# Kernel tuning notes

Measured on AMD Instinct MI355X. Metric: run time of the kernel, lower is better.

The kernel has to match this reference:

```python
import jax, jax.numpy as jnp
import numpy as np

N = 50000      # nodes (single node type 'tx')
E = 400000     # edges per edge type ('fwd' and 'rev')
F_IN = 128     # input feature dim
F = 128        # cfg.gnn.dim_inner
H = 8          # attention heads
D = F // H     # per-head dim
L = 2          # cfg.gnn.layers_mp
C = 2          # dim_out (fraud logits)


def setup_inputs() -> dict:
    key = jax.random.key(0)
    k = jax.random.split(key, 12)
    f32 = jnp.float32
    g = lambda kk, sh, fan: jax.random.normal(kk, sh, f32) / np.float32(np.sqrt(fan))
    return dict(
        x=jax.random.normal(k[0], (N, F_IN), f32),
        edge_index_fwd=jax.random.randint(k[1], (2, E), 0, N),
        edge_index_rev=jax.random.randint(k[2], (2, E), 0, N),
        in_w=g(k[3], (F_IN, F), F_IN),
        in_b=jnp.zeros((F,), f32),
        kqv_w=g(k[4], (L, F, 3 * F), F),
        kqv_b=jnp.zeros((L, 3 * F), f32),
        krel_w=g(k[5], (L, 2, H, D, D), D),
        vrel_w=g(k[6], (L, 2, H, D, D), D),
        p_rel=jnp.ones((L, 2, H), f32),
        out_w=g(k[7], (L, F, F), F),
        out_b=jnp.zeros((L, F), f32),
        skip=jnp.ones((L,), f32),
        head_w=g(k[8], (F, C), F),
        head_b=jnp.zeros((C,), f32),
    )


def reference(x, edge_index_fwd, edge_index_rev, in_w, in_b, kqv_w, kqv_b,
              krel_w, vrel_w, p_rel, out_w, out_b, skip, head_w, head_b):
    n = x.shape[0]
    ef, er = edge_index_fwd, edge_index_rev
    Ef, Er = ef.shape[1], er.shape[1]
    dst = jnp.concatenate([ef[1], er[1]])                 # [E_tot]
    scale = 1.0 / jnp.sqrt(jnp.asarray(D, x.dtype))

    h = x @ in_w + in_b                                   # in_proj['tx'], [N,F]
    for l in range(L):
        kqv = h @ kqv_w[l] + kqv_b[l]                     # [N,3F]
        k, q, v = jnp.split(kqv, 3, axis=1)
        k = k.reshape(n, H, D)
        q = q.reshape(n, H, D)
        v = v.reshape(n, H, D)
        # per-edge-type relation transforms (head-wise DxD, no bias)
        k_rel = jnp.einsum('nhd,ehdf->enhf', k, krel_w[l])  # [2,N,H,D]
        v_rel = jnp.einsum('nhd,ehdf->enhf', v, vrel_w[l])
        # gather src features per edge type, concatenate edge types
        k_j = jnp.concatenate([k_rel[0][ef[0]], k_rel[1][er[0]]], axis=0)  # [E_tot,H,D]
        v_j = jnp.concatenate([v_rel[0][ef[0]], v_rel[1][er[0]]], axis=0)
        p_e = jnp.concatenate([jnp.broadcast_to(p_rel[l, 0], (Ef, H)),
                               jnp.broadcast_to(p_rel[l, 1], (Er, H))], axis=0)
        q_i = q[dst]                                       # [E_tot,H,D]
        alpha = jnp.einsum('ehd,ehd->eh', q_i, k_j) * p_e * scale
        # segment softmax over all incoming edges of each dst node
        m = jax.ops.segment_max(alpha, dst, num_segments=n)
        ex = jnp.exp(alpha - m[dst])
        denom = jax.ops.segment_sum(ex, dst, num_segments=n)
        w = ex / (denom[dst] + 1e-16)                      # [E_tot,H]
        agg = jax.ops.segment_sum(w[:, :, None] * v_j, dst,
                                  num_segments=n).reshape(n, F)
        a = jax.nn.gelu(agg, approximate=False) @ out_w[l] + out_b[l]
        g = jax.nn.sigmoid(skip[l])
        h = jax.nn.relu(g * a + (1.0 - g) * h)             # skip + act(dropout=0)
    return h @ head_w + head_b                             # logits [N,C]
```

## Files before the change

kernel.cpp:

```cpp
#include <hip/hip_runtime.h>
#include <math.h>

typedef short short8 __attribute__((ext_vector_type(8)));
typedef float f32x4 __attribute__((ext_vector_type(4)));

__device__ __forceinline__ unsigned short f2bf(float f){
    unsigned u = __float_as_uint(f);
    unsigned r = u + 0x7fffu + ((u >> 16) & 1u);
    return (unsigned short)(r >> 16);
}
__device__ __forceinline__ float bf2f(unsigned short s){
    return __uint_as_float((unsigned)s << 16);
}

__global__ void k_count(const int* __restrict__ ef, const int* __restrict__ er,
                        int* __restrict__ deg, int Ef, int Er)
{
    int Etot = Ef + Er;
    for (int e = blockIdx.x*blockDim.x + threadIdx.x; e < Etot; e += gridDim.x*blockDim.x) {
        int dst = (e < Ef) ? ef[Ef + e] : er[Er + (e - Ef)];
        atomicAdd(&deg[dst], 1);
    }
}

__global__ void k_chunk_sums(const int* __restrict__ deg, int* __restrict__ csum, int n)
{
    __shared__ int s[256];
    int t = threadIdx.x, i = blockIdx.x*256 + t;
    s[t] = (i < n) ? deg[i] : 0;
    __syncthreads();
    for (int off = 128; off > 0; off >>= 1) {
        if (t < off) s[t] += s[t + off];
        __syncthreads();
    }
    if (t == 0) csum[blockIdx.x] = s[0];
}

__global__ void k_scan_chunks(int* __restrict__ csum, int nch)
{
    __shared__ int s[1024];
    int t = threadIdx.x;
    int v = (t < nch) ? csum[t] : 0;
    s[t] = v; __syncthreads();
    for (int off = 1; off < 1024; off <<= 1) {
        int u = (t >= off) ? s[t - off] : 0;
        __syncthreads();
        s[t] += u;
        __syncthreads();
    }
    if (t < nch) csum[t] = s[t] - v;
}

__global__ void k_rowstart(const int* __restrict__ deg, const int* __restrict__ csum,
                           int* __restrict__ row_start, int* __restrict__ cursor, int n)
{
    __shared__ int s[256];
    int t = threadIdx.x, i = blockIdx.x*256 + t;
    int d = (i < n) ? deg[i] : 0;
    s[t] = d; __syncthreads();
    for (int off = 1; off < 256; off <<= 1) {
        int u = (t >= off) ? s[t - off] : 0;
        __syncthreads();
        s[t] += u;
        __syncthreads();
    }
    if (i <= n) {
        int rs = csum[blockIdx.x] + s[t] - d;
        row_start[i] = rs;
        cursor[i] = rs;
    }
}

__global__ void k_fill(const int* __restrict__ ef, const int* __restrict__ er,
                       int* __restrict__ cursor, unsigned* __restrict__ srcs,
                       int Ef, int Er, int n_nodes)
{
    int Etot = Ef + Er;
    if (blockIdx.x == 0 && threadIdx.x < 8) srcs[Etot + threadIdx.x] = 0;
    for (int e = blockIdx.x*blockDim.x + threadIdx.x; e < Etot; e += gridDim.x*blockDim.x) {
        int src, dst, tt;
        if (e < Ef) { src = ef[e]; dst = ef[Ef + e]; tt = 0; }
        else { int e2 = e - Ef; src = er[e2]; dst = er[Er + e2]; tt = 1; }
        int pos = atomicAdd(&cursor[dst], 1);
        srcs[pos] = (unsigned)(tt*n_nodes + src)*32u;
    }
}

__global__ void k_setup(const float* __restrict__ kqv_w, const float* __restrict__ kqv_b,
                        const float* __restrict__ krel_w, const float* __restrict__ vrel_w,
                        const float* __restrict__ p_rel, const float* __restrict__ out_w,
                        const float* __restrict__ out_b, const float* __restrict__ in_w,
                        const float* __restrict__ x, const float* __restrict__ head_b,
                        unsigned short* __restrict__ WcT, float* __restrict__ biasc,
                        unsigned short* __restrict__ WoT, float* __restrict__ biaso,
                        unsigned short* __restrict__ WiT, unsigned short* __restrict__ x16,
                        int* __restrict__ deg, float* __restrict__ logits, int n_nodes)
{
    const int N0 = 2*129*640;
    const int N1 = N0 + 2*129*128;
    const int N2 = N1 + 128*128;
    const long long N3 = (long long)N2 + (long long)n_nodes*32;
    const long long N4 = N3 + n_nodes;
    const long long N5 = N4 + 2*n_nodes;

    for (long long idx = (long long)blockIdx.x*blockDim.x + threadIdx.x; idx < N5;
         idx += (long long)gridDim.x*blockDim.x) {
        if (idx < N0) {
            int i = (int)idx;
            int l = i / (129*640);
            int rem = i % (129*640);
            int r = rem / 640, c = rem % 640;
            float val;
            if (c < 128) {
                val = (r < 128) ? kqv_w[((size_t)l*128 + r)*384 + 128 + c]
                                : kqv_b[l*384 + 128 + c];
            } else {
                int c2 = c - 128;
                int tt = c2 >> 8;
                int cc = c2 & 255;
                int f = cc >> 1;
                int part = cc & 1;
                int hh = f >> 4, fd = f & 15;
                const float* rw = (part == 0 ? krel_w : vrel_w)
                                  + (((size_t)(l*2 + tt)*8 + hh)*16)*16 + fd;
                int base_col = (part == 0 ? 0 : 256) + hh*16;
                float s = 0.f;
                #pragma unroll
                for (int d = 0; d < 16; ++d) {
                    float a = (r < 128) ? kqv_w[((size_t)l*128 + r)*384 + base_col + d]
                                        : kqv_b[l*384 + base_col + d];
                    s += a * rw[d*16];
                }
                if (part == 0) s *= p_rel[(l*2 + tt)*8 + hh] * 0.25f * 1.4426950408889634f;
                val = s;
            }
            if (r < 128) WcT[((size_t)l*640 + c)*128 + r] = f2bf(val);
            else         biasc[l*640 + c] = val;
        } else if (idx < N1) {
            int i = (int)(idx - N0);
            int l = i / (129*128);
            int rem = i % (129*128);
            int r = rem / 128, c = rem % 128;
            if (r < 128) WoT[((size_t)l*128 + c)*128 + r] = f2bf(out_w[((size_t)l*128 + r)*128 + c]);
            else         biaso[l*128 + c] = out_b[l*128 + c];
        } else if (idx < N2) {
            int i = (int)(idx - N1);
            int r = i >> 7, c = i & 127;
            WiT[(size_t)c*128 + r] = f2bf(in_w[(size_t)r*128 + c]);
        } else if (idx < N3) {
            long long i = idx - N2;
            float4 v = *(const float4*)&x[i*4];
            uint2 w;
            w.x = (unsigned)f2bf(v.x) | ((unsigned)f2bf(v.y) << 16);
            w.y = (unsigned)f2bf(v.z) | ((unsigned)f2bf(v.w) << 16);
            *(uint2*)&x16[i*4] = w;
        } else if (idx < N4) {
            deg[idx - N3] = 0;
        } else {
            long long i = idx - N4;
            logits[i] = head_b[i & 1];
        }
    }
}

__global__ __launch_bounds__(256) void k_mfma(
    const unsigned short* __restrict__ A16, const unsigned short* __restrict__ WT,
    const float* __restrict__ biasc, unsigned short* __restrict__ q16,
    unsigned short* __restrict__ h16, unsigned* __restrict__ kv,
    const float* __restrict__ skip, const float* __restrict__ hw,
    float* __restrict__ logits, int l,
    int n_nodes, int R, int C, int mode)
{
    __shared__ uint4 As[64*16];
    __shared__ uint4 Ws[64*16];
    int b = blockIdx.x;
    int xcd = b & 7, jj = b >> 3;
    int r_t = (jj / C)*8 + xcd;
    int c_t = jj % C;
    if (r_t >= R) return;
    int n0 = r_t*64, c0 = c_t*64;
    int t = threadIdx.x;

    #pragma unroll
    for (int it = 0; it < 4; ++it) {
        int gi = t + it*256;
        int m = gi >> 4, g = gi & 15;
        uint4 a = *(const uint4*)&A16[((size_t)(n0 + m)*16 + g)*8];
        As[m*16 + (g ^ (m & 15))] = a;
    }
    #pragma unroll
    for (int it = 0; it < 4; ++it) {
        int gi = t + it*256;
        int cw = gi >> 4, g = gi & 15;
        uint4 wv = *(const uint4*)&WT[((size_t)(c0 + cw)*16 + g)*8];
        Ws[cw*16 + (g ^ (cw & 15))] = wv;
    }
    __syncthreads();

    int lane = t & 63, w = t >> 6;
    int lm = lane & 15, quad = lane >> 4;
    f32x4 acc[4];
    #pragma unroll
    for (int i = 0; i < 4; ++i) { acc[i][0]=0.f; acc[i][1]=0.f; acc[i][2]=0.f; acc[i][3]=0.f; }

    #pragma unroll
    for (int chunk = 0; chunk < 4; ++chunk) {
        int gq = chunk*4 + quad;
        short8 bfrag = *(const short8*)&Ws[(w*16 + lm)*16 + (gq ^ lm)];
        #pragma unroll
        for (int i = 0; i < 4; ++i) {
            short8 afrag = *(const short8*)&As[(i*16 + lm)*16 + (gq ^ lm)];
            acc[i] = __builtin_amdgcn_mfma_f32_16x16x32_bf16(afrag, bfrag, acc[i], 0, 0, 0);
        }
    }

    int c = c0 + w*16 + lm;
    float bc = biasc[c];
    bool even = (lane & 1) == 0;
    if (mode == 3) {
        float g = 1.f/(1.f + expf(-skip[l]));
        float hw0 = hw[c*2], hw1 = hw[c*2 + 1];
        #pragma unroll
        for (int i = 0; i < 4; ++i) {
            #pragma unroll
            for (int rr = 0; rr < 4; ++rr) {
                int m = n0 + i*16 + quad*4 + rr;
                float nv = 0.f;
                if (m < n_nodes) {
                    float hv = bf2f(h16[(size_t)m*128 + c]);
                    nv = fmaxf(g*(acc[i][rr] + bc) + (1.f - g)*hv, 0.f);
                }
                float p0 = nv*hw0, p1 = nv*hw1;
                p0 += __shfl_xor(p0, 1); p1 += __shfl_xor(p1, 1);
                p0 += __shfl_xor(p0, 2); p1 += __shfl_xor(p1, 2);
                p0 += __shfl_xor(p0, 4); p1 += __shfl_xor(p1, 4);
                p0 += __shfl_xor(p0, 8); p1 += __shfl_xor(p1, 8);
                if (lm == 0 && m < n_nodes) {
                    atomicAdd(&logits[m*2],     p0);
                    atomicAdd(&logits[m*2 + 1], p1);
                }
            }
        }
    } else if (mode == 2) {
        float g = 1.f/(1.f + expf(-skip[l]));
        unsigned* dst = (unsigned*)h16;
        #pragma unroll
        for (int i = 0; i < 4; ++i) {
            #pragma unroll
            for (int rr = 0; rr < 4; ++rr) {
                int m = n0 + i*16 + quad*4 + rr;
                float hv = (m < n_nodes) ? bf2f(h16[(size_t)m*128 + c]) : 0.f;
                float nv = fmaxf(g*(acc[i][rr] + bc) + (1.f - g)*hv, 0.f);
                float other = __shfl_xor(nv, 1);
                if (even && m < n_nodes)
                    dst[(size_t)m*64 + (c >> 1)] =
                        (unsigned)f2bf(nv) | ((unsigned)f2bf(other) << 16);
            }
        }
    } else if (mode == 0) {
        unsigned* dst = (unsigned*)h16;
        #pragma unroll
        for (int i = 0; i < 4; ++i) {
            #pragma unroll
            for (int rr = 0; rr < 4; ++rr) {
                int m = n0 + i*16 + quad*4 + rr;
                float nv = acc[i][rr] + bc;
                float other = __shfl_xor(nv, 1);
                if (even && m < n_nodes)
                    dst[(size_t)m*64 + (c >> 1)] =
                        (unsigned)f2bf(nv) | ((unsigned)f2bf(other) << 16);
            }
        }
    } else if (c0 < 128) {
        unsigned* dst = (unsigned*)q16;
        #pragma unroll
        for (int i = 0; i < 4; ++i) {
            #pragma unroll
            for (int rr = 0; rr < 4; ++rr) {
                float val = acc[i][rr] + bc;
                float other = __shfl_xor(val, 1);
                int m = n0 + i*16 + quad*4 + rr;
                if (even && m < n_nodes)
                    dst[(size_t)m*64 + (c >> 1)] =
                        (unsigned)f2bf(val) | ((unsigned)f2bf(other) << 16);
            }
        }
    } else {
        int c2 = c - 128;
        int tt = c2 >> 8;
        int f = (c2 & 255) >> 1;
        unsigned* dst = kv + (size_t)tt*n_nodes*128;
        #pragma unroll
        for (int i = 0; i < 4; ++i) {
            #pragma unroll
            for (int rr = 0; rr < 4; ++rr) {
                float val = acc[i][rr] + bc;
                float other = __shfl_xor(val, 1);
                int m = n0 + i*16 + quad*4 + rr;
                if (even && m < n_nodes) {
                    unsigned wd = ((unsigned)f2bf(val) << 16) | (unsigned)f2bf(other);
                    dst[(size_t)m*128 + f] = wd;
                }
            }
        }
    }
}

__global__ __launch_bounds__(256) void k_attn(
    const unsigned* __restrict__ srcs, const int* __restrict__ row_start,
    const uint4* __restrict__ kv, const unsigned short* __restrict__ q16,
    unsigned short* __restrict__ qa16, int n_nodes)
{
    int lane = threadIdx.x & 31;
    int n = blockIdx.x*8 + (threadIdx.x >> 5);
    if (n >= n_nodes) return;
    uint2 qp = *(const uint2*)&q16[(size_t)n*128 + lane*4];
    float4 q4;
    q4.x = __uint_as_float(qp.x << 16);
    q4.y = __uint_as_float(qp.x & 0xffff0000u);
    q4.z = __uint_as_float(qp.y << 16);
    q4.w = __uint_as_float(qp.y & 0xffff0000u);
    int s = row_start[n], e = row_start[n + 1];

    const uint4* kvl = kv + lane;

    float lsum = 0.f;
    float4 a = make_float4(0.f, 0.f, 0.f, 0.f);

    unsigned sv0 = srcs[s],     sv1 = srcs[s + 1];
    unsigned sv2 = srcs[s + 2], sv3 = srcs[s + 3];
    uint4 w0 = kvl[sv0], w1 = kvl[sv1], w2 = kvl[sv2], w3 = kvl[sv3];

    int pos = s;

#define ATT_PAIR(wA, wB)                                                       \
    {                                                                          \
        float d0 = __uint_as_float(wA.x & 0xffff0000u)*q4.x                    \
                 + __uint_as_float(wA.y & 0xffff0000u)*q4.y                    \
                 + __uint_as_float(wA.z & 0xffff0000u)*q4.z                    \
                 + __uint_as_float(wA.w & 0xffff0000u)*q4.w;                   \
        float d1 = __uint_as_float(wB.x & 0xffff0000u)*q4.x                    \
                 + __uint_as_float(wB.y & 0xffff0000u)*q4.y                    \
                 + __uint_as_float(wB.z & 0xffff0000u)*q4.z                    \
                 + __uint_as_float(wB.w & 0xffff0000u)*q4.w;                   \
        d0 += __shfl_xor(d0, 1); d1 += __shfl_xor(d1, 1);                      \
        d0 += __shfl_xor(d0, 2); d1 += __shfl_xor(d1, 2);                      \
        float wt0 = exp2f(d0), wt1 = exp2f(d1);                                \
        lsum += wt0 + wt1;                                                     \
        a.x += wt0*__uint_as_float(wA.x << 16);                                \
        a.y += wt0*__uint_as_float(wA.y << 16);                                \
        a.z += wt0*__uint_as_float(wA.z << 16);                                \
        a.w += wt0*__uint_as_float(wA.w << 16);                                \
        a.x += wt1*__uint_as_float(wB.x << 16);                                \
        a.y += wt1*__uint_as_float(wB.y << 16);                                \
        a.z += wt1*__uint_as_float(wB.z << 16);                                \
        a.w += wt1*__uint_as_float(wB.w << 16);                                \
    }

#define ATT_ONE(wA)                                                            \
    {                                                                          \
        float d = __uint_as_float(wA.x & 0xffff0000u)*q4.x                     \
                + __uint_as_float(wA.y & 0xffff0000u)*q4.y                     \
                + __uint_as_float(wA.z & 0xffff0000u)*q4.z                     \
                + __uint_as_float(wA.w & 0xffff0000u)*q4.w;                    \
        d += __shfl_xor(d, 1);                                                 \
        d += __shfl_xor(d, 2);                                                 \
        float wt = exp2f(d);                                                   \
        lsum += wt;                                                            \
        a.x += wt*__uint_as_float(wA.x << 16);                                 \
        a.y += wt*__uint_as_float(wA.y << 16);                                 \
        a.z += wt*__uint_as_float(wA.z << 16);                                 \
        a.w += wt*__uint_as_float(wA.w << 16);                                 \
    }

    for (; pos + 3 < e; pos += 4) {
        unsigned p0 = srcs[pos + 4], p1 = srcs[pos + 5];
        ATT_PAIR(w0, w1);
        w0 = kvl[p0]; w1 = kvl[p1];
        unsigned p2 = srcs[pos + 6], p3 = srcs[pos + 7];
        ATT_PAIR(w2, w3);
        w2 = kvl[p2]; w3 = kvl[p3];
    }
    int rem = e - pos;
    if (rem > 0) {
        ATT_ONE(w0);
        if (rem > 1) ATT_ONE(w1);
        if (rem > 2) ATT_ONE(w2);
    }
#undef ATT_PAIR
#undef ATT_ONE

    float inv = 1.f/(lsum + 1e-16f);
    float x0 = a.x*inv, x1 = a.y*inv, x2 = a.z*inv, x3 = a.w*inv;
    float g0 = 0.5f*x0*(1.f + erff(x0*0.70710678118654752f));
    float g1 = 0.5f*x1*(1.f + erff(x1*0.70710678118654752f));
    float g2 = 0.5f*x2*(1.f + erff(x2*0.70710678118654752f));
    float g3 = 0.5f*x3*(1.f + erff(x3*0.70710678118654752f));
    uint2 pk;
    pk.x = (unsigned)f2bf(g0) | ((unsigned)f2bf(g1) << 16);
    pk.y = (unsigned)f2bf(g2) | ((unsigned)f2bf(g3) << 16);
    *(uint2*)&qa16[(size_t)n*128 + lane*4] = pk;
}

extern "C" void kernel_launch(void* const* d_in, const int* in_sizes, int n_in,
                              void* d_out, int out_size, void* d_ws, size_t ws_size,
                              hipStream_t stream)
{
    const float* x      = (const float*)d_in[0];
    const int*   ef     = (const int*)d_in[1];
    const int*   er     = (const int*)d_in[2];
    const float* in_w   = (const float*)d_in[3];
    const float* in_b   = (const float*)d_in[4];
    const float* kqv_w  = (const float*)d_in[5];
    const float* kqv_b  = (const float*)d_in[6];
    const float* krel_w = (const float*)d_in[7];
    const float* vrel_w = (const float*)d_in[8];
    const float* p_rel  = (const float*)d_in[9];
    const float* out_w  = (const float*)d_in[10];
    const float* out_b  = (const float*)d_in[11];
    const float* skip   = (const float*)d_in[12];
    const float* head_w = (const float*)d_in[13];
    const float* head_b = (const float*)d_in[14];
    float* out = (float*)d_out;

    int n_nodes = in_sizes[0] / 128;
    int Ef = in_sizes[1] / 2, Er = in_sizes[2] / 2;
    int Etot = Ef + Er;
    int nch = (n_nodes + 255)/256;
    int ntile = (n_nodes + 63)/64;
    int npad = ntile*64;

    float* p = (float*)d_ws;
    unsigned* kv = (unsigned*)p; p += (size_t)2*n_nodes*128;
    unsigned short* h16  = (unsigned short*)p; p += (size_t)npad*128/2;
    unsigned short* q16  = (unsigned short*)p; p += (size_t)npad*128/2;
    unsigned short* qa16 = (unsigned short*)p; p += (size_t)npad*128/2;
    unsigned short* x16  = (unsigned short*)p; p += (size_t)npad*128/2;
    unsigned short* WiT = (unsigned short*)p; p += (size_t)(128*128)/2;
    unsigned short* WcT = (unsigned short*)p; p += (size_t)(2*640*128)/2;
    float* biasc = p; p += 2*640;
    unsigned short* WoT = (unsigned short*)p; p += (size_t)(2*128*128)/2;
    float* biaso = p; p += 2*128;
    int* deg       = (int*)p;      p += n_nodes;
    int* csum      = (int*)p;      p += 1024;
    int* row_start = (int*)p;      p += n_nodes + 1;
    int* cursor    = (int*)p;      p += n_nodes + 1;
    unsigned* srcs = (unsigned*)p; p += Etot + 8;

    int Rg = (ntile + 7)/8;

    k_setup<<<7500, 256, 0, stream>>>(kqv_w, kqv_b, krel_w, vrel_w, p_rel, out_w, out_b,
                                      in_w, x, head_b, WcT, biasc, WoT, biaso, WiT, x16,
                                      deg, out, n_nodes);
    k_count<<<1024, 256, 0, stream>>>(ef, er, deg, Ef, Er);
    k_chunk_sums<<<nch, 256, 0, stream>>>(deg, csum, n_nodes);
    k_scan_chunks<<<1, 1024, 0, stream>>>(csum, nch);
    k_rowstart<<<(n_nodes + 256)/256, 256, 0, stream>>>(deg, csum, row_start, cursor, n_nodes);
    k_fill<<<1024, 256, 0, stream>>>(ef, er, cursor, srcs, Ef, Er, n_nodes);

    k_mfma<<<Rg*8*2, 256, 0, stream>>>(x16, WiT, in_b, nullptr, h16, kv, skip,
                                       head_w, out, 0, n_nodes, ntile, 2, 0);
    for (int l = 0; l < 2; ++l) {
        k_mfma<<<Rg*8*10, 256, 0, stream>>>(h16, WcT + (size_t)l*640*128,
                                            biasc + l*640, q16, nullptr, kv, skip,
                                            head_w, out, l, n_nodes, ntile, 10, 1);
        k_attn<<<(n_nodes + 7)/8, 256, 0, stream>>>(srcs, row_start,
                                                    (const uint4*)kv, q16, qa16, n_nodes);
        int omode = (l == 1) ? 3 : 2;
        k_mfma<<<Rg*8*2, 256, 0, stream>>>(qa16, WoT + (size_t)l*128*128,
                                           biaso + l*128, nullptr, h16, kv, skip,
                                           head_w, out, l, n_nodes, ntile, 2, omode);
    }
}
```

Baseline: 432.3 us.

## Build CSR with per-block dst-range LDS atomics instead of global atomics

```diff
diff --git a/kernel.cpp b/kernel.cpp
--- a/kernel.cpp
+++ b/kernel.cpp
@@ -13,13 +13,48 @@
     return __uint_as_float((unsigned)s << 16);
 }
 
-__global__ void k_count(const int* __restrict__ ef, const int* __restrict__ er,
-                        int* __restrict__ deg, int Ef, int Er)
-{
+__global__ __launch_bounds__(512) void k_count_r(
+    const int* __restrict__ ef, const int* __restrict__ er,
+    int* __restrict__ deg, int Ef, int Er, int n_nodes, int rng)
+{
+    __shared__ int cnt[640];
+    int lo = blockIdx.x*rng;
+    int m = min(rng, n_nodes - lo);
+    if (m <= 0) return;
+    for (int i = threadIdx.x; i < m; i += 512) cnt[i] = 0;
+    __syncthreads();
     int Etot = Ef + Er;
-    for (int e = blockIdx.x*blockDim.x + threadIdx.x; e < Etot; e += gridDim.x*blockDim.x) {
+    for (int e = threadIdx.x; e < Etot; e += 512) {
         int dst = (e < Ef) ? ef[Ef + e] : er[Er + (e - Ef)];
-        atomicAdd(&deg[dst], 1);
+        unsigned r = (unsigned)(dst - lo);
+        if (r < (unsigned)m) atomicAdd(&cnt[r], 1);
+    }
+    __syncthreads();
+    for (int i = threadIdx.x; i < m; i += 512) deg[lo + i] = cnt[i];
+}
+
+__global__ __launch_bounds__(512) void k_fill_r(
+    const int* __restrict__ ef, const int* __restrict__ er,
+    const int* __restrict__ row_start, unsigned* __restrict__ srcs,
+    int Ef, int Er, int n_nodes, int rng)
+{
+    __shared__ int cur[640];
+    int Etot = Ef + Er;
+    if (blockIdx.x == 0 && threadIdx.x < 8) srcs[Etot + threadIdx.x] = 0;
+    int lo = blockIdx.x*rng;
+    int m = min(rng, n_nodes - lo);
+    if (m <= 0) return;
+    for (int i = threadIdx.x; i < m; i += 512) cur[i] = row_start[lo + i];
+    __syncthreads();
+    for (int e = threadIdx.x; e < Etot; e += 512) {
+        int src, dst, tt;
+        if (e < Ef) { src = ef[e]; dst = ef[Ef + e]; tt = 0; }
+        else { int e2 = e - Ef; src = er[e2]; dst = er[Er + e2]; tt = 1; }
+        unsigned r = (unsigned)(dst - lo);
+        if (r < (unsigned)m) {
+            int pos = atomicAdd(&cur[r], 1);
+            srcs[pos] = (unsigned)(tt*n_nodes + src)*32u;
+        }
     }
 }
 
@@ -52,7 +87,7 @@
 }
 
 __global__ void k_rowstart(const int* __restrict__ deg, const int* __restrict__ csum,
-                           int* __restrict__ row_start, int* __restrict__ cursor, int n)
+                           int* __restrict__ row_start, int n)
 {
     __shared__ int s[256];
     int t = threadIdx.x, i = blockIdx.x*256 + t;
@@ -64,26 +99,7 @@
         s[t] += u;
         __syncthreads();
     }
-    if (i <= n) {
-        int rs = csum[blockIdx.x] + s[t] - d;
-        row_start[i] = rs;
-        cursor[i] = rs;
-    }
-}
-
-__global__ void k_fill(const int* __restrict__ ef, const int* __restrict__ er,
-                       int* __restrict__ cursor, unsigned* __restrict__ srcs,
-                       int Ef, int Er, int n_nodes)
-{
-    int Etot = Ef + Er;
-    if (blockIdx.x == 0 && threadIdx.x < 8) srcs[Etot + threadIdx.x] = 0;
-    for (int e = blockIdx.x*blockDim.x + threadIdx.x; e < Etot; e += gridDim.x*blockDim.x) {
-        int src, dst, tt;
-        if (e < Ef) { src = ef[e]; dst = ef[Ef + e]; tt = 0; }
-        else { int e2 = e - Ef; src = er[e2]; dst = er[Er + e2]; tt = 1; }
-        int pos = atomicAdd(&cursor[dst], 1);
-        srcs[pos] = (unsigned)(tt*n_nodes + src)*32u;
-    }
+    if (i <= n) row_start[i] = csum[blockIdx.x] + s[t] - d;
 }
 
 __global__ void k_setup(const float* __restrict__ kqv_w, const float* __restrict__ kqv_b,
@@ -94,16 +110,15 @@
                         unsigned short* __restrict__ WcT, float* __restrict__ biasc,
                         unsigned short* __restrict__ WoT, float* __restrict__ biaso,
                         unsigned short* __restrict__ WiT, unsigned short* __restrict__ x16,
-                        int* __restrict__ deg, float* __restrict__ logits, int n_nodes)
+                        float* __restrict__ logits, int n_nodes)
 {
     const int N0 = 2*129*640;
     const int N1 = N0 + 2*129*128;
     const int N2 = N1 + 128*128;
     const long long N3 = (long long)N2 + (long long)n_nodes*32;
-    const long long N4 = N3 + n_nodes;
-    const long long N5 = N4 + 2*n_nodes;
-
-    for (long long idx = (long long)blockIdx.x*blockDim.x + threadIdx.x; idx < N5;
+    const long long N4 = N3 + 2*n_nodes;
+
+    for (long long idx = (long long)blockIdx.x*blockDim.x + threadIdx.x; idx < N4;
          idx += (long long)gridDim.x*blockDim.x) {
         if (idx < N0) {
             int i = (int)idx;
@@ -154,10 +169,8 @@
             w.x = (unsigned)f2bf(v.x) | ((unsigned)f2bf(v.y) << 16);
             w.y = (unsigned)f2bf(v.z) | ((unsigned)f2bf(v.w) << 16);
             *(uint2*)&x16[i*4] = w;
-        } else if (idx < N4) {
-            deg[idx - N3] = 0;
         } else {
-            long long i = idx - N4;
+            long long i = idx - N3;
             logits[i] = head_b[i & 1];
         }
     }
@@ -444,19 +457,20 @@
     int* deg       = (int*)p;      p += n_nodes;
     int* csum      = (int*)p;      p += 1024;
     int* row_start = (int*)p;      p += n_nodes + 1;
-    int* cursor    = (int*)p;      p += n_nodes + 1;
     unsigned* srcs = (unsigned*)p; p += Etot + 8;
 
     int Rg = (ntile + 7)/8;
+    int NB = (n_nodes + 639)/640;
+    int rng = (n_nodes + NB - 1)/NB;
 
     k_setup<<<7500, 256, 0, stream>>>(kqv_w, kqv_b, krel_w, vrel_w, p_rel, out_w, out_b,
                                       in_w, x, head_b, WcT, biasc, WoT, biaso, WiT, x16,
-                                      deg, out, n_nodes);
-    k_count<<<1024, 256, 0, stream>>>(ef, er, deg, Ef, Er);
+                                      out, n_nodes);
+    k_count_r<<<NB, 512, 0, stream>>>(ef, er, deg, Ef, Er, n_nodes, rng);
     k_chunk_sums<<<nch, 256, 0, stream>>>(deg, csum, n_nodes);
     k_scan_chunks<<<1, 1024, 0, stream>>>(csum, nch);
-    k_rowstart<<<(n_nodes + 256)/256, 256, 0, stream>>>(deg, csum, row_start, cursor, n_nodes);
-    k_fill<<<1024, 256, 0, stream>>>(ef, er, cursor, srcs, Ef, Er, n_nodes);
+    k_rowstart<<<(n_nodes + 256)/256, 256, 0, stream>>>(deg, csum, row_start, n_nodes);
+    k_fill_r<<<NB, 512, 0, stream>>>(ef, er, row_start, srcs, Ef, Er, n_nodes, rng);
 
     k_mfma<<<Rg*8*2, 256, 0, stream>>>(x16, WiT, in_b, nullptr, h16, kv, skip,
                                        head_w, out, 0, n_nodes, ntile, 2, 0);
```

After: 1.405 ms. 225% more time.
